# Kernel tuning notes

Hardware: AMD Instinct MI355X
Metric: run time of the kernel (lower is better)

The kernel has to match this reference:

```python
import jax, jax.numpy as jnp
import numpy as np

N = 2_000_000
IN_DIM = 1
HID = 64
NUM_SEG = 2048


def setup_inputs() -> dict:
    key = jax.random.key(0)
    ks = jax.random.split(key, 8)
    x = jax.random.normal(ks[0], (N, IN_DIM), dtype=jnp.float32)
    batch = jnp.sort(jax.random.randint(ks[1], (N,), 0, NUM_SEG, dtype=jnp.int64))
    s1 = 1.0 / np.sqrt(IN_DIM)
    s2 = 1.0 / np.sqrt(HID)
    W1 = jax.random.uniform(ks[2], (HID, IN_DIM), jnp.float32, -s1, s1)
    b1 = jax.random.uniform(ks[3], (HID,), jnp.float32, -s1, s1)
    W2 = jax.random.uniform(ks[4], (HID, HID), jnp.float32, -s2, s2)
    b2 = jax.random.uniform(ks[5], (HID,), jnp.float32, -s2, s2)
    W3 = jax.random.uniform(ks[6], (1, HID), jnp.float32, -s2, s2)
    b3 = jax.random.uniform(ks[7], (1,), jnp.float32, -s2, s2)
    return {"x": x, "batch": batch, "W1": W1, "b1": b1, "W2": W2, "b2": b2, "W3": W3, "b3": b3}


def reference(x, batch, W1, b1, W2, b2, W3, b3):
    batch = batch.astype(jnp.int32)
    h = jax.nn.relu(x @ W1.T + b1)          # [N, HID]
    h = jax.nn.relu(h @ W2.T + b2)          # [N, HID]
    pooled = jax.ops.segment_sum(h, batch, num_segments=NUM_SEG)  # [NUM_SEG, HID]
    counts = jax.ops.segment_sum(jnp.ones((h.shape[0],), h.dtype), batch, num_segments=NUM_SEG)
    pooled = pooled / jnp.maximum(counts, 1.0)[:, None]  # segment mean
    weights = jax.nn.relu((pooled @ W3.T + b3)[:, 0])    # [NUM_SEG]
    return weights[batch]                    # broadcast back to points [N]
```

## Files before the change

### kernel.cpp

```cpp
#include <hip/hip_runtime.h>
#include <math.h>

#define NSEG 2048
#define ROW 65
#define N2D (65 * ROW)
#define SCAN_PPT 8

__global__ __launch_bounds__(256) void k_pre_scan(
    const float* __restrict__ W1, const float* __restrict__ b1,
    const float* __restrict__ W2, const float* __restrict__ b2,
    const float* __restrict__ W3, const int* __restrict__ batch,
    float* __restrict__ bpg, float* __restrict__ knots, float2* __restrict__ coef,
    int* __restrict__ seg_start, int* __restrict__ seg_end, int n)
{
    __shared__ float bps[64];
    __shared__ float w2s[64 * 65];
    __shared__ float sc_[64], sda[64], sdb[64];
    const int tid = threadIdx.x;

    if (blockIdx.x >= 65) {
        int bid2 = blockIdx.x - 65;
        int base = bid2 * (256 * SCAN_PPT) + tid * SCAN_PPT;
        if (base >= n) return;
        const int4* bp = (const int4*)(batch + base);
        int4 a4 = bp[0], b4 = bp[1];
        int ss[SCAN_PPT] = {a4.x, a4.y, a4.z, a4.w, b4.x, b4.y, b4.z, b4.w};
        int prev = (base > 0) ? batch[base - 1] : -1;
#pragma unroll
        for (int p = 0; p < SCAN_PPT; ++p) {
            int u = (p == 0) ? prev : ss[p - 1];
            int v = ss[p];
            if (v != u) {
                int i = base + p;
                for (int s = (u > 0 ? u : 0); s < v; ++s) seg_end[s] = i;
                for (int s = u + 1; s <= v; ++s) seg_start[s] = i;
            }
        }
        if (base + SCAN_PPT >= n) {
            int u = ss[SCAN_PPT - 1];
            for (int s = u; s < NSEG; ++s) seg_end[s] = n;
            for (int s = u + 1; s < NSEG; ++s) seg_start[s] = n;
        }
        return;
    }

    const int k = blockIdx.x;
    const int lane = tid & 63;

    if (tid < 64) {
        float w1l = W1[lane], b1l = b1[lane];
        float t = (w1l != 0.0f) ? (-b1l / w1l) : 3.0e38f;
        int r = 0;
        for (int l = 0; l < 64; ++l) {
            float o = __shfl(t, l);
            r += (o < t) || (o == t && l < lane);
        }
        bps[r] = t;
    }
    for (int i = tid; i < 4096; i += 256)
        w2s[(i >> 6) * 65 + (i & 63)] = W2[i];
    __syncthreads();
    if (k == 0 && tid < 64) bpg[lane] = bps[lane];

    float a0 = 0.0f, b0 = 0.0f;
    if (tid < 64) {
        float lof = (k == 0) ? (bps[0] - 1.0f) : bps[k - 1];
        float hif = (k == 64) ? (bps[63] + 1.0f) : bps[k];
        float xm = lof + 0.5f * (hif - lof);
        float a = 0.0f, b = b2[lane];
        for (int j = 0; j < 64; ++j) {
            float w1 = W1[j];
            if (w1 * xm + b1[j] > 0.0f) {
                float w2 = w2s[lane * 65 + j];
                a += w2 * w1;
                b += w2 * b1[j];
            }
        }

        float w3 = W3[lane];
        float lo = (k == 0) ? -INFINITY : bps[k - 1];
        float hi = (k == 64) ? INFINITY : bps[k];
        float c = INFINITY, da = 0.0f, db = 0.0f;
        if (a != 0.0f) {
            float cc = -b / a;
            if (cc > lo && cc < hi) {
                float s = (a > 0.0f) ? 1.0f : -1.0f;
                c = cc; da = s * w3 * a; db = s * w3 * b;
            }
        }
        bool act;
        if (k == 0) act = (a < 0.0f) || (a == 0.0f && b > 0.0f);
        else { float v = a * lo + b; act = (v > 0.0f) || (v == 0.0f && a > 0.0f); }
        a0 = act ? w3 * a : 0.0f;
        b0 = act ? w3 * b : 0.0f;
        for (int d = 32; d; d >>= 1) { a0 += __shfl_xor(a0, d); b0 += __shfl_xor(b0, d); }

        int rank = 0;
        for (int l = 0; l < 64; ++l) {
            float o = __shfl(c, l);
            rank += (o < c) || (o == c && l < lane);
        }
        sc_[rank] = c; sda[rank] = da; sdb[rank] = db;
    }
    __syncthreads();
    if (tid < 64) {
        float cs = sc_[lane], das = sda[lane], dbs = sdb[lane];
        for (int d = 1; d < 64; d <<= 1) {
            float ta = __shfl_up(das, d);
            float tb = __shfl_up(dbs, d);
            if (lane >= d) { das += ta; dbs += tb; }
        }
        knots[k * ROW + lane] = cs;
        if (lane == 0) coef[k * ROW] = make_float2(a0, b0);
        coef[k * ROW + lane + 1] = make_float2(a0 + das, b0 + dbs);
    }
}

__global__ __launch_bounds__(256) void k_eval_out(
    const float* __restrict__ x,
    const int* __restrict__ seg_start, const int* __restrict__ seg_end,
    const float* __restrict__ bpg, const float* __restrict__ knots2d,
    const float2* __restrict__ coef2d,
    const float* __restrict__ b3, float* __restrict__ out)
{
    __shared__ float bps_s[64];
    __shared__ float T2_s[N2D];
    __shared__ double wsum[4];
    __shared__ float w_s;
    const int tid = threadIdx.x;
    const int s = blockIdx.x;

    const int start = seg_start[s];
    const int end   = seg_end[s];

    if (tid < 64) bps_s[tid] = bpg[tid];
    for (int i = tid; i < N2D; i += 256) T2_s[i] = knots2d[i];
    __syncthreads();
    if (start >= end) return;

    double acc = 0.0;
    for (int i = start + tid; i < end; i += 256) {
        float xv = x[i];
        int k = 0;
#pragma unroll
        for (int ofs = 32; ofs >= 1; ofs >>= 1)
            if (bps_s[k + ofs - 1] <= xv) k += ofs;
        k += (k < 64 && bps_s[k] <= xv) ? 1 : 0;
        const int kb = k * ROW;
        int j = 0;
#pragma unroll
        for (int ofs = 32; ofs >= 1; ofs >>= 1)
            if (T2_s[kb + j + ofs - 1] <= xv) j += ofs;
        j += (j < 64 && T2_s[kb + j] <= xv) ? 1 : 0;
        float2 ab = coef2d[kb + j];
        acc += (double)fmaf(ab.x, xv, ab.y);
    }

    for (int d = 32; d; d >>= 1) acc += __shfl_down(acc, d);
    if ((tid & 63) == 0) wsum[tid >> 6] = acc;
    __syncthreads();
    if (tid == 0) {
        double tot = wsum[0] + wsum[1] + wsum[2] + wsum[3];
        double mean = tot / (double)(end - start);
        w_s = fmaxf((float)(mean + (double)b3[0]), 0.0f);
    }
    __syncthreads();
    const float w = w_s;
    for (int i = start + tid; i < end; i += 256) out[i] = w;
}

extern "C" void kernel_launch(void* const* d_in, const int* in_sizes, int n_in,
                              void* d_out, int out_size, void* d_ws, size_t ws_size,
                              hipStream_t stream)
{
    const float* x   = (const float*)d_in[0];
    const int* batch = (const int*)d_in[1];
    const float* W1 = (const float*)d_in[2];
    const float* b1 = (const float*)d_in[3];
    const float* W2 = (const float*)d_in[4];
    const float* b2 = (const float*)d_in[5];
    const float* W3 = (const float*)d_in[6];
    const float* b3 = (const float*)d_in[7];
    float* out = (float*)d_out;
    const int n = in_sizes[0];

    char* ws = (char*)d_ws;
    int*    seg_start= (int*)ws;
    int*    seg_end  = (int*)(ws + 8192);
    float*  bpg      = (float*)(ws + 16384);
    float*  knots2d  = (float*)(ws + 16640);
    float2* coef2d   = (float2*)(ws + 33552);

    const int scanBlocks = (n + 256 * SCAN_PPT - 1) / (256 * SCAN_PPT);
    k_pre_scan<<<65 + scanBlocks, 256, 0, stream>>>(
        W1, b1, W2, b2, W3, batch, bpg, knots2d, coef2d,
        seg_start, seg_end, n);
    k_eval_out<<<NSEG, 256, 0, stream>>>(x, seg_start, seg_end, bpg,
                                         knots2d, coef2d, b3, out);
}
```

Before: 27.04 us.

## Replace segment-boundary scan pass with per-block wave-parallel binary search

Removes the scan blocks that read the whole batch array to build segment start/end tables. Each eval block instead finds its segment bounds with a 64-ary ballot-based lower-bound search over sorted batch, two waves in parallel, while the other waves load the knot tables. This drops a full pass over the index array but adds serialized global-load latency at the start of each block.

```diff
diff --git a/kernel.cpp b/kernel.cpp
--- a/kernel.cpp
+++ b/kernel.cpp
@@ -4,46 +4,17 @@
 #define NSEG 2048
 #define ROW 65
 #define N2D (65 * ROW)
-#define SCAN_PPT 8
 
-__global__ __launch_bounds__(256) void k_pre_scan(
+__global__ __launch_bounds__(256) void k_pre_ab(
     const float* __restrict__ W1, const float* __restrict__ b1,
     const float* __restrict__ W2, const float* __restrict__ b2,
-    const float* __restrict__ W3, const int* __restrict__ batch,
-    float* __restrict__ bpg, float* __restrict__ knots, float2* __restrict__ coef,
-    int* __restrict__ seg_start, int* __restrict__ seg_end, int n)
+    const float* __restrict__ W3,
+    float* __restrict__ bpg, float* __restrict__ knots, float2* __restrict__ coef)
 {
     __shared__ float bps[64];
     __shared__ float w2s[64 * 65];
     __shared__ float sc_[64], sda[64], sdb[64];
     const int tid = threadIdx.x;
-
-    if (blockIdx.x >= 65) {
-        int bid2 = blockIdx.x - 65;
-        int base = bid2 * (256 * SCAN_PPT) + tid * SCAN_PPT;
-        if (base >= n) return;
-        const int4* bp = (const int4*)(batch + base);
-        int4 a4 = bp[0], b4 = bp[1];
-        int ss[SCAN_PPT] = {a4.x, a4.y, a4.z, a4.w, b4.x, b4.y, b4.z, b4.w};
-        int prev = (base > 0) ? batch[base - 1] : -1;
-#pragma unroll
-        for (int p = 0; p < SCAN_PPT; ++p) {
-            int u = (p == 0) ? prev : ss[p - 1];
-            int v = ss[p];
-            if (v != u) {
-                int i = base + p;
-                for (int s = (u > 0 ? u : 0); s < v; ++s) seg_end[s] = i;
-                for (int s = u + 1; s <= v; ++s) seg_start[s] = i;
-            }
-        }
-        if (base + SCAN_PPT >= n) {
-            int u = ss[SCAN_PPT - 1];
-            for (int s = u; s < NSEG; ++s) seg_end[s] = n;
-            for (int s = u + 1; s < NSEG; ++s) seg_start[s] = n;
-        }
-        return;
-    }
-
     const int k = blockIdx.x;
     const int lane = tid & 63;
 
@@ -116,26 +87,55 @@
     }
 }
 
+__device__ __forceinline__ int wave_lower_bound(const int* __restrict__ batch,
+                                                int n, int target, int lane)
+{
+    long long lo = -1, hi = n;
+    while (hi - lo > 65) {
+        long long d = hi - lo;
+        long long q = lo + 1 + (((d - 1) * lane) >> 6);
+        int v = batch[q];
+        unsigned long long m = __ballot(v < target);
+        int c = (int)__popcll(m);
+        long long nlo = (c > 0) ? (lo + 1 + (((d - 1) * (c - 1)) >> 6)) : lo;
+        long long nhi = (c < 64) ? (lo + 1 + (((d - 1) * c) >> 6)) : hi;
+        lo = nlo; hi = nhi;
+    }
+    long long q = lo + 1 + lane;
+    int v = (q < hi) ? batch[q] : 0x7fffffff;
+    unsigned long long m = __ballot(v < target);
+    return (int)(lo + 1 + __popcll(m));
+}
+
 __global__ __launch_bounds__(256) void k_eval_out(
-    const float* __restrict__ x,
-    const int* __restrict__ seg_start, const int* __restrict__ seg_end,
+    const float* __restrict__ x, const int* __restrict__ batch,
     const float* __restrict__ bpg, const float* __restrict__ knots2d,
     const float2* __restrict__ coef2d,
-    const float* __restrict__ b3, float* __restrict__ out)
+    const float* __restrict__ b3, float* __restrict__ out, int n)
 {
     __shared__ float bps_s[64];
     __shared__ float T2_s[N2D];
+    __shared__ int bounds_s[2];
     __shared__ double wsum[4];
     __shared__ float w_s;
     const int tid = threadIdx.x;
+    const int wv = tid >> 6;
+    const int lane = tid & 63;
     const int s = blockIdx.x;
 
-    const int start = seg_start[s];
-    const int end   = seg_end[s];
-
-    if (tid < 64) bps_s[tid] = bpg[tid];
-    for (int i = tid; i < N2D; i += 256) T2_s[i] = knots2d[i];
+    if (wv == 0) {
+        int st = wave_lower_bound(batch, n, s, lane);
+        if (lane == 0) bounds_s[0] = st;
+    } else if (wv == 1) {
+        int en = wave_lower_bound(batch, n, s + 1, lane);
+        if (lane == 0) bounds_s[1] = en;
+    } else {
+        if (wv == 2 && lane < 64) bps_s[lane] = bpg[lane];
+        for (int i = tid - 128; i < N2D; i += 128) T2_s[i] = knots2d[i];
+    }
     __syncthreads();
+    const int start = bounds_s[0];
+    const int end   = bounds_s[1];
     if (start >= end) return;
 
     double acc = 0.0;
@@ -185,16 +185,11 @@
     const int n = in_sizes[0];
 
     char* ws = (char*)d_ws;
-    int*    seg_start= (int*)ws;
-    int*    seg_end  = (int*)(ws + 8192);
-    float*  bpg      = (float*)(ws + 16384);
-    float*  knots2d  = (float*)(ws + 16640);
-    float2* coef2d   = (float2*)(ws + 33552);
+    float*  bpg      = (float*)ws;
+    float*  knots2d  = (float*)(ws + 256);
+    float2* coef2d   = (float2*)(ws + 17168);
 
-    const int scanBlocks = (n + 256 * SCAN_PPT - 1) / (256 * SCAN_PPT);
-    k_pre_scan<<<65 + scanBlocks, 256, 0, stream>>>(
-        W1, b1, W2, b2, W3, batch, bpg, knots2d, coef2d,
-        seg_start, seg_end, n);
-    k_eval_out<<<NSEG, 256, 0, stream>>>(x, seg_start, seg_end, bpg,
-                                         knots2d, coef2d, b3, out);
+    k_pre_ab<<<65, 256, 0, stream>>>(W1, b1, W2, b2, W3, bpg, knots2d, coef2d);
+    k_eval_out<<<NSEG, 256, 0, stream>>>(x, batch, bpg, knots2d, coef2d,
+                                         b3, out, n);
 }
```

New measurement: 27.39 us. No clear change (+1.3%).
